# Optimization experiments

Measured on AMD Instinct MI355X. Metric: run time of the kernel, lower is better.

The kernel has to match this reference:

```python
import jax, jax.numpy as jnp
from jax import lax
import numpy as np

EPS = 1e-9

def squash(x):
    # squash along last axis: ||x||^2/(1+||x||^2) * x/||x||
    mag_sq = jnp.sum(x * x, axis=-1, keepdims=True)
    mag = jnp.sqrt(mag_sq + EPS)
    return mag_sq / (1.0 + mag_sq) * (x / (mag + EPS))

def setup_inputs() -> dict:
    key = jax.random.key(0)
    ks = jax.random.split(key, 4)
    x = jax.random.normal(ks[0], (64, 1, 64, 64), jnp.float32)
    conv1_w = jax.random.normal(ks[1], (64, 1, 5, 5), jnp.float32) * 0.1
    conv1_b = jnp.zeros((64,), jnp.float32)
    prim_w = jax.random.normal(ks[2], (64, 64, 9, 9), jnp.float32) * 0.05
    prim_b = jnp.zeros((64,), jnp.float32)
    # DigitCaps W: (num_routes=8*28*28, num_caps=10, out_dim=16, in_dim=8); torch uses randn
    W = jax.random.normal(ks[3], (6272, 10, 16, 8), jnp.float32)
    return {"x": x, "conv1_w": conv1_w, "conv1_b": conv1_b,
            "prim_w": prim_w, "prim_b": prim_b, "W": W}

def reference(x, conv1_w, conv1_b, prim_w, prim_b, W):
    dn = ("NCHW", "OIHW", "NCHW")
    # ConvLayer: conv(1->64, k5, pad2) + relu, spatial preserved
    h = lax.conv_general_dilated(x, conv1_w, (1, 1), [(2, 2), (2, 2)], dimension_numbers=dn)
    h = jax.nn.relu(h + conv1_b[None, :, None, None])
    # PrimaryCaps: 8 convs (64->8, k9, s2) fused as one 64-channel conv
    u = lax.conv_general_dilated(h, prim_w, (2, 2), "VALID", dimension_numbers=dn)
    u = u + prim_b[None, :, None, None]  # (B, 64, 28, 28)
    B, _, H, Wd = u.shape
    # (B, caps=8, dim=8, H, W) -> (B, caps, H, W, dim) -> (B, caps*H*W, 8)
    u = u.reshape(B, 8, 8, H, Wd).transpose(0, 1, 3, 4, 2).reshape(B, -1, 8)
    u = squash(u)
    # u_hat[b,n,o,i] = W[n,o,i,j] @ u[b,n,j]   (B, routes, 10, 16)
    u_hat = jnp.einsum("noij,bnj->bnoi", W, u)
    b_ij = jnp.zeros(u_hat.shape[:3], u_hat.dtype)  # (B, routes, 10)
    v = None
    for it in range(3):
        c = jax.nn.softmax(b_ij, axis=2)
        s = jnp.einsum("bno,bnoi->boi", c, u_hat)  # (B, 10, 16)
        v = squash(s)
        if it < 2:
            b_ij = b_ij + jnp.einsum("bnoi,boi->bno", u_hat, v)
    return v.reshape(B, -1)  # (B, 160)
```

## Files before the change

kernel.cpp:

```cpp
#include <hip/hip_runtime.h>
#include <math.h>

typedef unsigned short ushort_t;
typedef __attribute__((ext_vector_type(8))) short bf16x8;
typedef __attribute__((ext_vector_type(4))) float f32x4;
typedef __attribute__((ext_vector_type(8))) unsigned short us8;

typedef __attribute__((address_space(1))) unsigned int gu32;
typedef __attribute__((address_space(3))) unsigned int lu32;

__device__ __forceinline__ void gload16(const void* g, void* l) {
    __builtin_amdgcn_global_load_lds((const gu32*)g, (lu32*)l, 16, 0, 0);
}

__device__ __forceinline__ unsigned short f2bf(float f) {
    unsigned u = __float_as_uint(f);
    unsigned r = ((u >> 16) & 1u) + 0x7fffu;
    return (unsigned short)((u + r) >> 16);
}

#define HB_OFF    0ULL
#define WB_OFF    0ULL
#define WT2_OFF   8388608ULL
#define TMP_OFF   8554496ULL
#define UTB_OFF   11765760ULL
#define S_OFF     13371392ULL
#define V0_OFF    13381632ULL
#define V1_OFF    13391872ULL
#define PART_OFF  13402112ULL
#define PART2_OFF 21430272ULL

__global__ __launch_bounds__(256) void conv1_nhwc_kernel(const float* __restrict__ x,
                                                         const float* __restrict__ w,
                                                         const float* __restrict__ bias,
                                                         ushort_t* __restrict__ hb) {
    int t = blockIdx.x * 256 + threadIdx.x;
    int xx = t & 63, yy = (t >> 6) & 63, b = t >> 12;
    int cg = blockIdx.y;
    const float* xb = x + (size_t)b * 4096;
    float xv[25];
    #pragma unroll
    for (int ky = 0; ky < 5; ++ky) {
        int iy = yy + ky - 2;
        #pragma unroll
        for (int kx = 0; kx < 5; ++kx) {
            int ix = xx + kx - 2;
            bool ok = (iy >= 0 && iy < 64 && ix >= 0 && ix < 64);
            xv[ky * 5 + kx] = ok ? xb[iy * 64 + ix] : 0.f;
        }
    }
    us8 o;
    #pragma unroll
    for (int cc = 0; cc < 8; ++cc) {
        int c = cg * 8 + cc;
        float acc = bias[c];
        const float* wc = w + c * 25;
        #pragma unroll
        for (int k = 0; k < 25; ++k) acc = fmaf(xv[k], wc[k], acc);
        o[cc] = f2bf(fmaxf(acc, 0.f));
    }
    *(us8*)&hb[(size_t)t * 64 + cg * 8] = o;
}

__global__ __launch_bounds__(256) void wt2_transform_kernel(const float* __restrict__ pw,
                                                            ushort_t* __restrict__ wt2) {
    int t = blockIdx.x * 256 + threadIdx.x;
    int ic = t & 63, c = (t >> 6) & 63, p = t >> 12;
    wt2[t] = f2bf(pw[(size_t)(c * 64 + ic) * 81 + p]);
}

__global__ __launch_bounds__(256) void conv2_mfma_kernel(const ushort_t* __restrict__ hb,
                                                         const ushort_t* __restrict__ wt2,
                                                         const float* __restrict__ pb,
                                                         float* __restrict__ tmp) {
    __shared__ ushort_t As[2][4096];
    __shared__ ushort_t Bs[2][4096];

    int tid = threadIdx.x;
    int w = tid >> 6, lane = tid & 63;
    int m0 = blockIdx.x * 64;

    int srow = w * 16 + (lane >> 3);
    int srcchunk = (lane & 7) ^ ((lane >> 3) & 7);
    unsigned gbaseA[2];
    #pragma unroll
    for (int k = 0; k < 2; ++k) {
        int r = srow + k * 8;
        int m = m0 + r;
        int b = m / 784, pos = m % 784;
        int oy = pos / 28, ox = pos % 28;
        gbaseA[k] = ((unsigned)((b * 64 + 2 * oy) * 64 + 2 * ox)) * 64 + srcchunk * 8;
    }
    unsigned gbaseB[2] = { (unsigned)srow * 64 + srcchunk * 8,
                           (unsigned)(srow + 8) * 64 + srcchunk * 8 };

    int fr = lane & 15, fq = lane >> 4;
    int rlow = fr & 7;
    int c0 = (fq ^ rlow) * 8;
    int c1 = ((4 + fq) ^ rlow) * 8;
    int rowA = w * 16 + fr;
    int offA0 = rowA * 64 + c0, offA1 = rowA * 64 + c1;
    int offB0[4], offB1[4];
    #pragma unroll
    for (int jf = 0; jf < 4; ++jf) {
        int rowB = jf * 16 + fr;
        offB0[jf] = rowB * 64 + c0;
        offB1[jf] = rowB * 64 + c1;
    }

    f32x4 acc[4] = {};

    auto stage = [&](int p, int buf) {
        int ky = p / 9, kx = p % 9;
        unsigned koff = (unsigned)(ky * 4096 + kx * 64);
        unsigned boff = (unsigned)p * 4096;
        gload16(hb + gbaseA[0] + koff, &As[buf][w * 1024]);
        gload16(hb + gbaseA[1] + koff, &As[buf][w * 1024 + 512]);
        gload16(wt2 + boff + gbaseB[0], &Bs[buf][w * 1024]);
        gload16(wt2 + boff + gbaseB[1], &Bs[buf][w * 1024 + 512]);
    };

    stage(0, 0);
    __syncthreads();

    for (int p = 0; p < 81; ++p) {
        int cur = p & 1;
        const ushort_t* A = As[cur];
        const ushort_t* B = Bs[cur];
        bf16x8 a0 = *(const bf16x8*)&A[offA0];
        bf16x8 a1 = *(const bf16x8*)&A[offA1];
        bf16x8 b0[4], b1[4];
        #pragma unroll
        for (int jf = 0; jf < 4; ++jf) {
            b0[jf] = *(const bf16x8*)&B[offB0[jf]];
            b1[jf] = *(const bf16x8*)&B[offB1[jf]];
        }
        #pragma unroll
        for (int jf = 0; jf < 4; ++jf)
            acc[jf] = __builtin_amdgcn_mfma_f32_16x16x32_bf16(a0, b0[jf], acc[jf], 0, 0, 0);
        #pragma unroll
        for (int jf = 0; jf < 4; ++jf)
            acc[jf] = __builtin_amdgcn_mfma_f32_16x16x32_bf16(a1, b1[jf], acc[jf], 0, 0, 0);
        if (p < 80) stage(p + 1, cur ^ 1);
        __syncthreads();
    }

    #pragma unroll
    for (int jf = 0; jf < 4; ++jf) {
        int n = jf * 16 + fr;
        float bv = pb[n];
        #pragma unroll
        for (int reg = 0; reg < 4; ++reg) {
            int m = w * 16 + fq * 4 + reg;
            tmp[(size_t)(m0 + m) * 64 + n] = acc[jf][reg] + bv;
        }
    }
}

__global__ __launch_bounds__(256) void squash_u_kernel(const float* __restrict__ tmp,
                                                       ushort_t* __restrict__ utb) {
    int idx = blockIdx.x * 256 + threadIdx.x;
    int b = idx & 63;
    int n = idx >> 6;
    int caps = n / 784, pos = n % 784;
    const float* tp = tmp + ((size_t)b * 784 + pos) * 64 + caps * 8;
    float v[8]; float msq = 0.f;
    #pragma unroll
    for (int j = 0; j < 8; ++j) { v[j] = tp[j]; msq = fmaf(v[j], v[j], msq); }
    float mag = sqrtf(msq + 1e-9f);
    float sc = msq / (1.f + msq) / (mag + 1e-9f);
    us8 o;
    #pragma unroll
    for (int j = 0; j < 8; ++j) o[j] = f2bf(v[j] * sc);
    *(us8*)&utb[(size_t)idx * 8] = o;
}

__global__ __launch_bounds__(256) void wb_kernel(const float* __restrict__ W,
                                                 ushort_t* __restrict__ Wb) {
    int t = blockIdx.x * 256 + threadIdx.x;
    const float* src = W + (size_t)t * 8;
    us8 o;
    #pragma unroll
    for (int j = 0; j < 8; ++j) o[j] = f2bf(src[j]);
    *(us8*)&Wb[(size_t)t * 8] = o;
}

#define RPB 8
template<int ITER>
__global__ __launch_bounds__(256) void routing5_kernel(const ushort_t* __restrict__ Wb,
                                                       const ushort_t* __restrict__ utb,
                                                       const float* __restrict__ v0,
                                                       const float* __restrict__ v1,
                                                       float* __restrict__ part) {
    __shared__ ushort_t Wl[RPB * 1280];
    __shared__ ushort_t Ul[RPB * 512];
    int tid = threadIdx.x;
    int lane = tid & 63;
    int wid = tid >> 6;
    int fr = lane & 15, fq = lane >> 4;
    int n0 = blockIdx.x * RPB;
    int b = wid * 16 + fr;

    {
        int w64 = wid * 64;
        const ushort_t* wsrc = Wb + (size_t)n0 * 1280;
        #pragma unroll
        for (int k = 0; k < 5; ++k)
            gload16(wsrc + (size_t)(k * 256 + tid) * 8, &Wl[(k * 256 + w64) * 8]);
        const ushort_t* usrc = utb + (size_t)n0 * 512;
        #pragma unroll
        for (int k = 0; k < 2; ++k)
            gload16(usrc + (size_t)(k * 256 + tid) * 8, &Ul[(k * 256 + w64) * 8]);
    }

    float vsum[40];
    if (ITER >= 1) {
        #pragma unroll
        for (int o = 0; o < 10; ++o) {
            f32x4 a = *(const f32x4*)&v0[b * 160 + o * 16 + fq * 4];
            if (ITER == 2) {
                f32x4 cc = *(const f32x4*)&v1[b * 160 + o * 16 + fq * 4];
                a = a + cc;
            }
            *(f32x4*)&vsum[o * 4] = a;
        }
    }

    __syncthreads();

    float sacc[40];
    #pragma unroll
    for (int q = 0; q < 40; ++q) sacc[q] = 0.f;

    const bf16x8 zf = {};
    const f32x4 zc = {};

    #pragma unroll 1
    for (int t = 0; t < RPB; ++t) {
        bf16x8 bfrag = zf;
        if (fq == 0) bfrag = *(const bf16x8*)&Ul[(t * 64 + b) * 8];

        f32x4 uh[10];
        #pragma unroll
        for (int o = 0; o < 10; ++o) {
            bf16x8 afrag = zf;
            if (fq == 0) afrag = *(const bf16x8*)&Wl[(t * 160 + o * 16 + fr) * 8];
            uh[o] = __builtin_amdgcn_mfma_f32_16x16x32_bf16(afrag, bfrag, zc, 0, 0, 0);
        }

        float c10[10];
        if (ITER >= 1) {
            float l[10];
            #pragma unroll
            for (int o = 0; o < 10; ++o) {
                float lo = uh[o][0] * vsum[o * 4] + uh[o][1] * vsum[o * 4 + 1] +
                           uh[o][2] * vsum[o * 4 + 2] + uh[o][3] * vsum[o * 4 + 3];
                lo += __shfl_xor(lo, 16);
                lo += __shfl_xor(lo, 32);
                l[o] = lo;
            }
            float m = l[0];
            #pragma unroll
            for (int o = 1; o < 10; ++o) m = fmaxf(m, l[o]);
            float sum = 0.f;
            #pragma unroll
            for (int o = 0; o < 10; ++o) { c10[o] = __expf(l[o] - m); sum += c10[o]; }
            float inv = 1.f / sum;
            #pragma unroll
            for (int o = 0; o < 10; ++o) c10[o] *= inv;
        }

        #pragma unroll
        for (int o = 0; o < 10; ++o) {
            float co = (ITER == 0) ? 1.f : c10[o];
            sacc[o * 4 + 0] = fmaf(co, uh[o][0], sacc[o * 4 + 0]);
            sacc[o * 4 + 1] = fmaf(co, uh[o][1], sacc[o * 4 + 1]);
            sacc[o * 4 + 2] = fmaf(co, uh[o][2], sacc[o * 4 + 2]);
            sacc[o * 4 + 3] = fmaf(co, uh[o][3], sacc[o * 4 + 3]);
        }
    }

    float* pp = part + (size_t)blockIdx.x * 10240;
    #pragma unroll
    for (int o = 0; o < 10; ++o)
        #pragma unroll
        for (int r = 0; r < 4; ++r)
            pp[(o * 16 + fq * 4 + r) * 64 + b] = sacc[o * 4 + r];
}

__global__ __launch_bounds__(256) void reduce_part1_kernel(const float* __restrict__ part,
                                                           float* __restrict__ part2) {
    int idx = blockIdx.x * 256 + threadIdx.x;
    int kc = blockIdx.y;
    const float* p = part + (size_t)kc * 49 * 10240 + idx;
    float a0 = 0.f, a1 = 0.f, a2 = 0.f, a3 = 0.f;
    #pragma unroll
    for (int k = 0; k < 48; k += 4) {
        a0 += p[(size_t)(k + 0) * 10240];
        a1 += p[(size_t)(k + 1) * 10240];
        a2 += p[(size_t)(k + 2) * 10240];
        a3 += p[(size_t)(k + 3) * 10240];
    }
    part2[kc * 10240 + idx] = ((a0 + a1) + (a2 + a3)) + p[48ULL * 10240];
}

__global__ __launch_bounds__(1024) void reduce_squash_kernel(const float* __restrict__ part2,
                                                             float scale,
                                                             float* __restrict__ v) {
    __shared__ float sv[16][64];
    int tid = threadIdx.x;
    int o = blockIdx.x;
    int i = tid >> 6, b = tid & 63;
    int idx = (o * 16 + i) * 64 + b;
    float a0 = 0.f, a1 = 0.f, a2 = 0.f, a3 = 0.f;
    #pragma unroll
    for (int k = 0; k < 16; k += 4) {
        a0 += part2[(k + 0) * 10240 + idx];
        a1 += part2[(k + 1) * 10240 + idx];
        a2 += part2[(k + 2) * 10240 + idx];
        a3 += part2[(k + 3) * 10240 + idx];
    }
    float s = ((a0 + a1) + (a2 + a3)) * scale;
    sv[i][b] = s * s;
    __syncthreads();
    float msq = 0.f;
    #pragma unroll
    for (int ii = 0; ii < 16; ++ii) msq += sv[ii][b];
    float mag = sqrtf(msq + 1e-9f);
    float sc = msq / (1.f + msq) / (mag + 1e-9f);
    v[b * 160 + o * 16 + i] = s * sc;
}

extern "C" void kernel_launch(void* const* d_in, const int* in_sizes, int n_in,
                              void* d_out, int out_size, void* d_ws, size_t ws_size,
                              hipStream_t stream) {
    const float* x  = (const float*)d_in[0];
    const float* w1 = (const float*)d_in[1];
    const float* b1 = (const float*)d_in[2];
    const float* pw = (const float*)d_in[3];
    const float* pb = (const float*)d_in[4];
    const float* W  = (const float*)d_in[5];
    float* out = (float*)d_out;
    float* ws  = (float*)d_ws;

    ushort_t* hb    = (ushort_t*)(ws + HB_OFF);
    ushort_t* Wb    = (ushort_t*)(ws + WB_OFF);
    ushort_t* wt2   = (ushort_t*)(ws + WT2_OFF);
    float*    tmp   = ws + TMP_OFF;
    ushort_t* utb   = (ushort_t*)(ws + UTB_OFF);
    float*    v0    = ws + V0_OFF;
    float*    v1    = ws + V1_OFF;
    float*    part  = ws + PART_OFF;
    float*    part2 = ws + PART2_OFF;

    conv1_nhwc_kernel<<<dim3(1024, 8), 256, 0, stream>>>(x, w1, b1, hb);
    wt2_transform_kernel<<<1296, 256, 0, stream>>>(pw, wt2);
    conv2_mfma_kernel<<<784, 256, 0, stream>>>(hb, wt2, pb, tmp);
    wb_kernel<<<3920, 256, 0, stream>>>(W, Wb);
    squash_u_kernel<<<1568, 256, 0, stream>>>(tmp, utb);

    routing5_kernel<0><<<784, 256, 0, stream>>>(Wb, utb, nullptr, nullptr, part);
    reduce_part1_kernel<<<dim3(40, 16), 256, 0, stream>>>(part, part2);
    reduce_squash_kernel<<<10, 1024, 0, stream>>>(part2, 0.1f, v0);

    routing5_kernel<1><<<784, 256, 0, stream>>>(Wb, utb, v0, nullptr, part);
    reduce_part1_kernel<<<dim3(40, 16), 256, 0, stream>>>(part, part2);
    reduce_squash_kernel<<<10, 1024, 0, stream>>>(part2, 1.f, v1);

    routing5_kernel<2><<<784, 256, 0, stream>>>(Wb, utb, v0, v1, part);
    reduce_part1_kernel<<<dim3(40, 16), 256, 0, stream>>>(part, part2);
    reduce_squash_kernel<<<10, 1024, 0, stream>>>(part2, 1.f, out);
}
```

Measured before the change: 296.8 us.

## Merge weight prep kernels, triple-buffer conv2, specialise routing iteration zero

Combines the two weight conversion kernels into one launch, with Wb moved to its own workspace region instead of aliasing hb. Replaces conv2's double buffering with a three-slot pipeline using explicit vmcnt waits and barriers so loads run further ahead of the MFMAs. Adds a dedicated iteration-0 routing kernel that computes uniform-coupling sums directly with MFMA, skipping softmax. Reshapes reduce_squash into 40 blocks of 256 threads. These changes add launch-level and memory-latency overlap at the cost of more LDS and hand-written synchronisation.

```diff
diff --git a/kernel.cpp b/kernel.cpp
--- a/kernel.cpp
+++ b/kernel.cpp
@@ -20,15 +20,14 @@
 }
 
 #define HB_OFF    0ULL
-#define WB_OFF    0ULL
 #define WT2_OFF   8388608ULL
 #define TMP_OFF   8554496ULL
 #define UTB_OFF   11765760ULL
-#define S_OFF     13371392ULL
 #define V0_OFF    13381632ULL
 #define V1_OFF    13391872ULL
 #define PART_OFF  13402112ULL
 #define PART2_OFF 21430272ULL
+#define WB2_OFF   21594112ULL
 
 __global__ __launch_bounds__(256) void conv1_nhwc_kernel(const float* __restrict__ x,
                                                          const float* __restrict__ w,
@@ -62,19 +61,32 @@
     *(us8*)&hb[(size_t)t * 64 + cg * 8] = o;
 }
 
-__global__ __launch_bounds__(256) void wt2_transform_kernel(const float* __restrict__ pw,
-                                                            ushort_t* __restrict__ wt2) {
-    int t = blockIdx.x * 256 + threadIdx.x;
-    int ic = t & 63, c = (t >> 6) & 63, p = t >> 12;
-    wt2[t] = f2bf(pw[(size_t)(c * 64 + ic) * 81 + p]);
+__global__ __launch_bounds__(256) void prep_weights_kernel(const float* __restrict__ pw,
+                                                           const float* __restrict__ W,
+                                                           ushort_t* __restrict__ wt2,
+                                                           ushort_t* __restrict__ Wb) {
+    int bid = blockIdx.x;
+    int tid = threadIdx.x;
+    if (bid < 1296) {
+        int t = bid * 256 + tid;
+        int ic = t & 63, c = (t >> 6) & 63, p = t >> 12;
+        wt2[t] = f2bf(pw[(size_t)(c * 64 + ic) * 81 + p]);
+    } else {
+        int t = (bid - 1296) * 256 + tid;
+        const float* src = W + (size_t)t * 8;
+        us8 o;
+        #pragma unroll
+        for (int j = 0; j < 8; ++j) o[j] = f2bf(src[j]);
+        *(us8*)&Wb[(size_t)t * 8] = o;
+    }
 }
 
 __global__ __launch_bounds__(256) void conv2_mfma_kernel(const ushort_t* __restrict__ hb,
                                                          const ushort_t* __restrict__ wt2,
                                                          const float* __restrict__ pb,
                                                          float* __restrict__ tmp) {
-    __shared__ ushort_t As[2][4096];
-    __shared__ ushort_t Bs[2][4096];
+    __shared__ ushort_t As[3][4096];
+    __shared__ ushort_t Bs[3][4096];
 
     int tid = threadIdx.x;
     int w = tid >> 6, lane = tid & 63;
@@ -110,23 +122,20 @@
 
     f32x4 acc[4] = {};
 
-    auto stage = [&](int p, int buf) {
+    auto stage = [&](int p) {
+        int slot = p % 3;
         int ky = p / 9, kx = p % 9;
         unsigned koff = (unsigned)(ky * 4096 + kx * 64);
         unsigned boff = (unsigned)p * 4096;
-        gload16(hb + gbaseA[0] + koff, &As[buf][w * 1024]);
-        gload16(hb + gbaseA[1] + koff, &As[buf][w * 1024 + 512]);
-        gload16(wt2 + boff + gbaseB[0], &Bs[buf][w * 1024]);
-        gload16(wt2 + boff + gbaseB[1], &Bs[buf][w * 1024 + 512]);
+        gload16(hb + gbaseA[0] + koff, &As[slot][w * 1024]);
+        gload16(hb + gbaseA[1] + koff, &As[slot][w * 1024 + 512]);
+        gload16(wt2 + boff + gbaseB[0], &Bs[slot][w * 1024]);
+        gload16(wt2 + boff + gbaseB[1], &Bs[slot][w * 1024 + 512]);
     };
 
-    stage(0, 0);
-    __syncthreads();
-
-    for (int p = 0; p < 81; ++p) {
-        int cur = p & 1;
-        const ushort_t* A = As[cur];
-        const ushort_t* B = Bs[cur];
+    auto tap = [&](int p) {
+        const ushort_t* A = As[p % 3];
+        const ushort_t* B = Bs[p % 3];
         bf16x8 a0 = *(const bf16x8*)&A[offA0];
         bf16x8 a1 = *(const bf16x8*)&A[offA1];
         bf16x8 b0[4], b1[4];
@@ -141,9 +150,31 @@
         #pragma unroll
         for (int jf = 0; jf < 4; ++jf)
             acc[jf] = __builtin_amdgcn_mfma_f32_16x16x32_bf16(a1, b1[jf], acc[jf], 0, 0, 0);
-        if (p < 80) stage(p + 1, cur ^ 1);
-        __syncthreads();
-    }
+    };
+
+    stage(0); stage(1); stage(2);
+
+    for (int p = 0; p < 78; ++p) {
+        asm volatile("s_waitcnt vmcnt(8)" ::: "memory");
+        __builtin_amdgcn_s_barrier();
+        __builtin_amdgcn_sched_barrier(0);
+        tap(p);
+        __builtin_amdgcn_sched_barrier(0);
+        __builtin_amdgcn_s_barrier();
+        stage(p + 3);
+    }
+    asm volatile("s_waitcnt vmcnt(8)" ::: "memory");
+    __builtin_amdgcn_s_barrier();
+    __builtin_amdgcn_sched_barrier(0);
+    tap(78);
+    asm volatile("s_waitcnt vmcnt(4)" ::: "memory");
+    __builtin_amdgcn_s_barrier();
+    __builtin_amdgcn_sched_barrier(0);
+    tap(79);
+    asm volatile("s_waitcnt vmcnt(0)" ::: "memory");
+    __builtin_amdgcn_s_barrier();
+    __builtin_amdgcn_sched_barrier(0);
+    tap(80);
 
     #pragma unroll
     for (int jf = 0; jf < 4; ++jf) {
@@ -175,17 +206,52 @@
     *(us8*)&utb[(size_t)idx * 8] = o;
 }
 
-__global__ __launch_bounds__(256) void wb_kernel(const float* __restrict__ W,
-                                                 ushort_t* __restrict__ Wb) {
-    int t = blockIdx.x * 256 + threadIdx.x;
-    const float* src = W + (size_t)t * 8;
-    us8 o;
-    #pragma unroll
-    for (int j = 0; j < 8; ++j) o[j] = f2bf(src[j]);
-    *(us8*)&Wb[(size_t)t * 8] = o;
-}
-
 #define RPB 8
+__global__ __launch_bounds__(256) void routing_iter0_kernel(const ushort_t* __restrict__ Wb,
+                                                            const ushort_t* __restrict__ utb,
+                                                            float* __restrict__ part) {
+    __shared__ ushort_t Wl[RPB * 1280];
+    __shared__ ushort_t Ul[RPB * 512];
+    int tid = threadIdx.x;
+    int lane = tid & 63;
+    int wid = tid >> 6;
+    int fr = lane & 15, fq = lane >> 4;
+    int n0 = blockIdx.x * RPB;
+
+    {
+        int w64 = wid * 64;
+        const ushort_t* wsrc = Wb + (size_t)n0 * 1280;
+        #pragma unroll
+        for (int k = 0; k < 5; ++k)
+            gload16(wsrc + (size_t)(k * 256 + tid) * 8, &Wl[(k * 256 + w64) * 8]);
+        const ushort_t* usrc = utb + (size_t)n0 * 512;
+        #pragma unroll
+        for (int k = 0; k < 2; ++k)
+            gload16(usrc + (size_t)(k * 256 + tid) * 8, &Ul[(k * 256 + w64) * 8]);
+    }
+    __syncthreads();
+
+    f32x4 s4[10] = {};
+    #pragma unroll
+    for (int g = 0; g < 2; ++g) {
+        int t = g * 4 + fq;
+        bf16x8 bfrag = *(const bf16x8*)&Ul[(t * 64 + wid * 16 + fr) * 8];
+        #pragma unroll
+        for (int o = 0; o < 10; ++o) {
+            bf16x8 afrag = *(const bf16x8*)&Wl[(t * 160 + o * 16 + fr) * 8];
+            s4[o] = __builtin_amdgcn_mfma_f32_16x16x32_bf16(afrag, bfrag, s4[o], 0, 0, 0);
+        }
+    }
+
+    float* pp = part + (size_t)blockIdx.x * 10240;
+    int b = wid * 16 + fr;
+    #pragma unroll
+    for (int o = 0; o < 10; ++o)
+        #pragma unroll
+        for (int r = 0; r < 4; ++r)
+            pp[(o * 16 + fq * 4 + r) * 64 + b] = s4[o][r];
+}
+
 template<int ITER>
 __global__ __launch_bounds__(256) void routing5_kernel(const ushort_t* __restrict__ Wb,
                                                        const ushort_t* __restrict__ utb,
@@ -214,16 +280,14 @@
     }
 
     float vsum[40];
-    if (ITER >= 1) {
-        #pragma unroll
-        for (int o = 0; o < 10; ++o) {
-            f32x4 a = *(const f32x4*)&v0[b * 160 + o * 16 + fq * 4];
-            if (ITER == 2) {
-                f32x4 cc = *(const f32x4*)&v1[b * 160 + o * 16 + fq * 4];
-                a = a + cc;
-            }
-            *(f32x4*)&vsum[o * 4] = a;
-        }
+    #pragma unroll
+    for (int o = 0; o < 10; ++o) {
+        f32x4 a = *(const f32x4*)&v0[b * 160 + o * 16 + fq * 4];
+        if (ITER == 2) {
+            f32x4 cc = *(const f32x4*)&v1[b * 160 + o * 16 + fq * 4];
+            a = a + cc;
+        }
+        *(f32x4*)&vsum[o * 4] = a;
     }
 
     __syncthreads();
@@ -249,7 +313,7 @@
         }
 
         float c10[10];
-        if (ITER >= 1) {
+        {
             float l[10];
             #pragma unroll
             for (int o = 0; o < 10; ++o) {
@@ -272,7 +336,7 @@
 
         #pragma unroll
         for (int o = 0; o < 10; ++o) {
-            float co = (ITER == 0) ? 1.f : c10[o];
+            float co = c10[o];
             sacc[o * 4 + 0] = fmaf(co, uh[o][0], sacc[o * 4 + 0]);
             sacc[o * 4 + 1] = fmaf(co, uh[o][1], sacc[o * 4 + 1]);
             sacc[o * 4 + 2] = fmaf(co, uh[o][2], sacc[o * 4 + 2]);
@@ -304,13 +368,14 @@
     part2[kc * 10240 + idx] = ((a0 + a1) + (a2 + a3)) + p[48ULL * 10240];
 }
 
-__global__ __launch_bounds__(1024) void reduce_squash_kernel(const float* __restrict__ part2,
-                                                             float scale,
-                                                             float* __restrict__ v) {
-    __shared__ float sv[16][64];
+__global__ __launch_bounds__(256) void reduce_squash_kernel(const float* __restrict__ part2,
+                                                            float scale,
+                                                            float* __restrict__ v) {
+    __shared__ float sv[16][17];
     int tid = threadIdx.x;
     int o = blockIdx.x;
-    int i = tid >> 6, b = tid & 63;
+    int i = tid >> 4, bl = tid & 15;
+    int b = blockIdx.y * 16 + bl;
     int idx = (o * 16 + i) * 64 + b;
     float a0 = 0.f, a1 = 0.f, a2 = 0.f, a3 = 0.f;
     #pragma unroll
@@ -321,11 +386,11 @@
         a3 += part2[(k + 3) * 10240 + idx];
     }
     float s = ((a0 + a1) + (a2 + a3)) * scale;
-    sv[i][b] = s * s;
+    sv[i][bl] = s * s;
     __syncthreads();
     float msq = 0.f;
     #pragma unroll
-    for (int ii = 0; ii < 16; ++ii) msq += sv[ii][b];
+    for (int ii = 0; ii < 16; ++ii) msq += sv[ii][bl];
     float mag = sqrtf(msq + 1e-9f);
     float sc = msq / (1.f + msq) / (mag + 1e-9f);
     v[b * 160 + o * 16 + i] = s * sc;
@@ -344,7 +409,6 @@
     float* ws  = (float*)d_ws;
 
     ushort_t* hb    = (ushort_t*)(ws + HB_OFF);
-    ushort_t* Wb    = (ushort_t*)(ws + WB_OFF);
     ushort_t* wt2   = (ushort_t*)(ws + WT2_OFF);
     float*    tmp   = ws + TMP_OFF;
     ushort_t* utb   = (ushort_t*)(ws + UTB_OFF);
@@ -352,22 +416,22 @@
     float*    v1    = ws + V1_OFF;
     float*    part  = ws + PART_OFF;
     float*    part2 = ws + PART2_OFF;
-
+    ushort_t* Wb    = (ushort_t*)(ws + WB2_OFF);
+
+    prep_weights_kernel<<<5216, 256, 0, stream>>>(pw, W, wt2, Wb);
     conv1_nhwc_kernel<<<dim3(1024, 8), 256, 0, stream>>>(x, w1, b1, hb);
-    wt2_transform_kernel<<<1296, 256, 0, stream>>>(pw, wt2);
     conv2_mfma_kernel<<<784, 256, 0, stream>>>(hb, wt2, pb, tmp);
-    wb_kernel<<<3920, 256, 0, stream>>>(W, Wb);
     squash_u_kernel<<<1568, 256, 0, stream>>>(tmp, utb);
 
-    routing5_kernel<0><<<784, 256, 0, stream>>>(Wb, utb, nullptr, nullptr, part);
+    routing_iter0_kernel<<<784, 256, 0, stream>>>(Wb, utb, part);
     reduce_part1_kernel<<<dim3(40, 16), 256, 0, stream>>>(part, part2);
-    reduce_squash_kernel<<<10, 1024, 0, stream>>>(part2, 0.1f, v0);
+    reduce_squash_kernel<<<dim3(10, 4), 256, 0, stream>>>(part2, 0.1f, v0);
 
     routing5_kernel<1><<<784, 256, 0, stream>>>(Wb, utb, v0, nullptr, part);
     reduce_part1_kernel<<<dim3(40, 16), 256, 0, stream>>>(part, part2);
-    reduce_squash_kernel<<<10, 1024, 0, stream>>>(part2, 1.f, v1);
+    reduce_squash_kernel<<<dim3(10, 4), 256, 0, stream>>>(part2, 1.f, v1);
 
     routing5_kernel<2><<<784, 256, 0, stream>>>(Wb, utb, v0, v1, part);
     reduce_part1_kernel<<<dim3(40, 16), 256, 0, stream>>>(part, part2);
-    reduce_squash_kernel<<<10, 1024, 0, stream>>>(part2, 1.f, out);
-}
+    reduce_squash_kernel<<<dim3(10, 4), 256, 0, stream>>>(part2, 1.f, out);
+}
```

After: 325.7 us. 1.1x slower.
